# Kernel tuning notes

Hardware: AMD Instinct MI355X
Metric: run time of the kernel (lower is better)

## Reference

```python
import jax, jax.numpy as jnp
import numpy as np

GAMMA = 5e-4
IN_DIM, HID = 512, 4096
N = HID  # batch must equal hidden_dim for classifier(gram) to type-check


def setup_inputs() -> dict:
    key = jax.random.key(0)
    ks = jax.random.split(key, 7)
    s = lambda fan_in: 1.0 / np.sqrt(fan_in)
    return {
        "x": jax.random.normal(ks[0], (N, IN_DIM), jnp.float32),
        "W1": jax.random.uniform(ks[1], (HID, IN_DIM), jnp.float32, -s(IN_DIM), s(IN_DIM)),
        "b1": jax.random.uniform(ks[2], (HID,), jnp.float32, -s(IN_DIM), s(IN_DIM)),
        "W2": jax.random.uniform(ks[3], (HID, HID), jnp.float32, -s(HID), s(HID)),
        "b2": jax.random.uniform(ks[4], (HID,), jnp.float32, -s(HID), s(HID)),
        "Wc": jax.random.uniform(ks[5], (1, HID), jnp.float32, -s(HID), s(HID)),
        "bc": jax.random.uniform(ks[6], (1,), jnp.float32, -s(HID), s(HID)),
    }


def reference(x, W1, b1, W2, b2, Wc, bc):
    h = jnp.tanh(x @ W1.T + b1)          # [N, HID]
    h = jnp.tanh(h @ W2.T + b2)          # [N, HID]
    # KernelLayer: support = h.detach() (first call), RBF gram via cdist+exp
    support = jax.lax.stop_gradient(h)   # [N, HID]
    sq = (jnp.sum(h * h, axis=1, keepdims=True)
          + jnp.sum(support * support, axis=1)[None, :]
          - 2.0 * (h @ support.T))       # [N, N] squared distances
    gram = jnp.exp(-GAMMA * sq)
    return gram @ Wc.T + bc              # [N, 1]
```

## Files before the change

kernel.cpp:

```cpp
#include <hip/hip_runtime.h>
#include <hip/hip_bf16.h>


#define NROWS 4096
#define HID   4096
#define INDIM 512
#define GAMMA_F 5e-4f

typedef float f32x4  __attribute__((ext_vector_type(4)));
typedef int   i32x4  __attribute__((ext_vector_type(4)));
typedef int   i32x8  __attribute__((ext_vector_type(8)));

#define BAR() asm volatile("s_barrier" ::: "memory")
#define SCALE1 0x7F7F7F7F

__device__ __forceinline__ unsigned char f2e4m3(float x) {
  unsigned int u = __float_as_uint(x);
  unsigned char s = (unsigned char)((u >> 24) & 0x80u);
  float a = fabsf(x);
  if (a >= 448.f) return s | 0x7E;
  if (a < 0.015625f) {
    int q = (int)rintf(a * 512.f);
    return s | (unsigned char)q;
  }
  unsigned int ua = u & 0x7fffffffu;
  ua += 0x7FFFFu + ((ua >> 20) & 1u);
  int e = (int)(ua >> 23) - 127;
  unsigned int m = (ua >> 20) & 7u;
  return s | (unsigned char)(((e + 7) << 3) | m);
}

__global__ void prep(const float* __restrict__ x, const float* __restrict__ W1,
                     const float* __restrict__ W2, const float* __restrict__ bc,
                     unsigned char* __restrict__ xq, unsigned char* __restrict__ w1q,
                     unsigned char* __restrict__ w2q,
                     float* __restrict__ out, float* __restrict__ norms) {
  const int gi = blockIdx.x * blockDim.x + threadIdx.x;
  if (gi < NROWS) { out[gi] = bc[0]; norms[gi] = 0.f; }
  const int NX  = NROWS * INDIM / 8;
  const int NW2 = HID * HID / 8;
  const int total = 2 * NX + NW2;
  const int stride = gridDim.x * blockDim.x;
  for (int i = gi; i < total; i += stride) {
    const float* src; unsigned char* dst; float sc; int j;
    if (i < NX)            { src = x;  dst = xq;  sc = 16.f;  j = i; }
    else if (i < 2 * NX)   { src = W1; dst = w1q; sc = 32.f;  j = i - NX; }
    else                   { src = W2; dst = w2q; sc = 128.f; j = i - 2 * NX; }
    float4 v0 = ((const float4*)src)[j * 2];
    float4 v1 = ((const float4*)src)[j * 2 + 1];
    unsigned int r0 = (unsigned int)f2e4m3(v0.x * sc)
                    | ((unsigned int)f2e4m3(v0.y * sc) << 8)
                    | ((unsigned int)f2e4m3(v0.z * sc) << 16)
                    | ((unsigned int)f2e4m3(v0.w * sc) << 24);
    unsigned int r1 = (unsigned int)f2e4m3(v1.x * sc)
                    | ((unsigned int)f2e4m3(v1.y * sc) << 8)
                    | ((unsigned int)f2e4m3(v1.z * sc) << 16)
                    | ((unsigned int)f2e4m3(v1.w * sc) << 24);
    uint2 o; o.x = r0; o.y = r1;
    ((uint2*)dst)[j] = o;
  }
}

__device__ __forceinline__ void gload16(const void* g, void* l) {
  __builtin_amdgcn_global_load_lds(
      (const __attribute__((address_space(1))) void*)g,
      (__attribute__((address_space(3))) void*)l, 16, 0, 0);
}

#define LDFRAG(dst, base0, off, RSTRIDE) do {                       \
    i32x4 lo_ = *(const i32x4*)((base0) + (off));                   \
    i32x4 hi_ = *(const i32x4*)((base0) + (RSTRIDE) + (off));       \
    dst = __builtin_shufflevector(lo_, hi_, 0, 1, 2, 3, 4, 5, 6, 7); } while (0)

#define MFMA16(d, a, b) \
    d = __builtin_amdgcn_mfma_scale_f32_16x16x128_f8f6f4( \
        a, b, d, 0, 0, 0, SCALE1, 0, SCALE1)

template <int EPI>
__global__ __launch_bounds__(512, 2)
void gemm256_fp8(const unsigned char* __restrict__ A, const unsigned char* __restrict__ B,
                 int K, int N,
                 const float* __restrict__ bias, unsigned char* __restrict__ Hout,
                 float* __restrict__ norms_out) {
  __shared__ __align__(16) unsigned char As[2][2][256 * 64];
  __shared__ __align__(16) unsigned char Bs[2][2][256 * 64];

  const int tid  = threadIdx.x;
  const int lane = tid & 63;
  const int wave = tid >> 6;
  const int wr = wave >> 2, wc = wave & 3;
  const int fr = lane & 15, fq = lane >> 4;

  const int nwg = gridDim.x;
  const int cpx = nwg >> 3;
  const int bid = blockIdx.x;
  const int swzb = (bid & 7) * cpx + (bid >> 3);
  const int nbx = N >> 8;
  const int brow = (swzb / nbx) << 8;
  const int bcol = (swzb % nbx) << 8;

  const unsigned char* ap[4]; const unsigned char* bp[4]; int ldq[4];
#pragma unroll
  for (int q = 0; q < 4; ++q) {
    int idx = q * 512 + tid;
    int h   = idx >> 10;
    int row = (idx >> 2) & 255;
    int c   = idx & 3;
    int gcol = ((((c ^ ((row >> 1) & 3)) << 1) | h) << 4);
    ap[q] = A + (size_t)(brow + row) * K + gcol;
    bp[q] = B + (size_t)(bcol + row) * K + gcol;
    ldq[q] = (q * 512 + wave * 64) * 16;
  }
#define STAGE_A(p, tt) do { int kk = (tt) * 128;              \
    gload16(ap[0] + kk, &As[p][0][0] + ldq[0]);               \
    gload16(ap[1] + kk, &As[p][0][0] + ldq[1]);               \
    gload16(ap[2] + kk, &As[p][0][0] + ldq[2]);               \
    gload16(ap[3] + kk, &As[p][0][0] + ldq[3]); } while (0)
#define STAGE_B(p, tt) do { int kk = (tt) * 128;              \
    gload16(bp[0] + kk, &Bs[p][0][0] + ldq[0]);               \
    gload16(bp[1] + kk, &Bs[p][0][0] + ldq[1]);               \
    gload16(bp[2] + kk, &Bs[p][0][0] + ldq[2]);               \
    gload16(bp[3] + kk, &Bs[p][0][0] + ldq[3]); } while (0)

  int aoff[8], boff[4];
#pragma unroll
  for (int mi = 0; mi < 8; ++mi) {
    int row = wr * 128 + mi * 16 + fr;
    aoff[mi] = row * 64 + ((fq ^ ((row >> 1) & 3)) << 4);
  }
#pragma unroll
  for (int nj = 0; nj < 4; ++nj) {
    int row = wc * 64 + nj * 16 + fr;
    boff[nj] = row * 64 + ((fq ^ ((row >> 1) & 3)) << 4);
  }

  const int NT = K >> 7;

  STAGE_A(0, 0); STAGE_B(0, 0);
  STAGE_A(1, 1); STAGE_B(1, 1);
  asm volatile("s_waitcnt vmcnt(8)" ::: "memory");
  BAR();

  f32x4 acc[8][4] = {};
  i32x8 afr[4], bfr[4];

  for (int t = 0; t < NT; ++t) {
    const int p = t & 1;
    int t2 = t + 2; if (t2 >= NT) t2 = NT - 1;

#pragma unroll
    for (int mi = 0; mi < 4; ++mi) LDFRAG(afr[mi], &As[p][0][0], aoff[mi], 16384);
#pragma unroll
    for (int nj = 0; nj < 4; ++nj) LDFRAG(bfr[nj], &Bs[p][0][0], boff[nj], 16384);
    asm volatile("s_waitcnt lgkmcnt(0)" ::: "memory");
    BAR();
    STAGE_B(p, t2);
    __builtin_amdgcn_sched_barrier(0);
    __builtin_amdgcn_s_setprio(1);
#pragma unroll
    for (int mi = 0; mi < 4; ++mi)
#pragma unroll
      for (int nj = 0; nj < 4; ++nj) MFMA16(acc[mi][nj], afr[mi], bfr[nj]);
    __builtin_amdgcn_s_setprio(0);

#pragma unroll
    for (int mi = 0; mi < 4; ++mi) LDFRAG(afr[mi], &As[p][0][0], aoff[4 + mi], 16384);
    asm volatile("s_waitcnt lgkmcnt(0)" ::: "memory");
    BAR();
    STAGE_A(p, t2);
    __builtin_amdgcn_sched_barrier(0);
    __builtin_amdgcn_s_setprio(1);
#pragma unroll
    for (int mi = 0; mi < 4; ++mi)
#pragma unroll
      for (int nj = 0; nj < 4; ++nj) MFMA16(acc[4 + mi][nj], afr[mi], bfr[nj]);
    __builtin_amdgcn_s_setprio(0);
    asm volatile("s_waitcnt vmcnt(8)" ::: "memory");
    BAR();
  }
  asm volatile("s_waitcnt vmcnt(0)" ::: "memory");

  const float rescale = (EPI == 0) ? (1.f / 512.f) : (1.f / 1024.f);
  float bv[4];
#pragma unroll
  for (int nj = 0; nj < 4; ++nj) bv[nj] = bias[bcol + wc * 64 + nj * 16 + fr];
#pragma unroll
  for (int mi = 0; mi < 8; ++mi) {
    int row0 = brow + wr * 128 + mi * 16 + fq * 4;
#pragma unroll
    for (int rr = 0; rr < 4; ++rr) {
      float ns = 0.f;
#pragma unroll
      for (int nj = 0; nj < 4; ++nj) {
        int col = bcol + wc * 64 + nj * 16 + fr;
        float v = tanhf(acc[mi][nj][rr] * rescale + bv[nj]);
        Hout[(size_t)(row0 + rr) * N + col] = f2e4m3(8.f * v);
        if (EPI == 2) ns += v * v;
      }
      if (EPI == 2) {
        ns += __shfl_xor(ns, 1);
        ns += __shfl_xor(ns, 2);
        ns += __shfl_xor(ns, 4);
        ns += __shfl_xor(ns, 8);
        if (fr == 0) atomicAdd(&norms_out[row0 + rr], ns);
      }
    }
  }
#undef STAGE_A
#undef STAGE_B
}

__global__ __launch_bounds__(256, 2)
void gram_tri(const unsigned char* __restrict__ H, int K,
              const float* __restrict__ norms, const float* __restrict__ Wc,
              float* __restrict__ out) {
  __shared__ __align__(16) unsigned char As[2][2][128 * 64];
  __shared__ __align__(16) unsigned char Bs[2][2][128 * 64];

  const int tid  = threadIdx.x;
  const int lane = tid & 63;
  const int wave = tid >> 6;
  const int wr = wave >> 1, wc = wave & 1;
  const int fr = lane & 15, fq = lane >> 4;

  const int bid = blockIdx.x;
  const int swzb = (bid & 7) * 66 + (bid >> 3);
  int I = (int)((sqrtf(8.0f * (float)swzb + 1.0f) - 1.0f) * 0.5f);
  while ((I + 1) * (I + 2) / 2 <= swzb) ++I;
  while (I * (I + 1) / 2 > swzb) --I;
  const int J = swzb - I * (I + 1) / 2;
  const int brow = I << 7, bcol = J << 7;
  const bool diag = (I == J);

  const unsigned char* ap[4]; const unsigned char* bp[4]; int ldq[4];
#pragma unroll
  for (int q = 0; q < 4; ++q) {
    int idx = q * 256 + tid;
    int h   = idx >> 9;
    int row = (idx >> 2) & 127;
    int c   = idx & 3;
    int gcol = ((((c ^ ((row >> 1) & 3)) << 1) | h) << 4);
    ap[q] = H + (size_t)(brow + row) * K + gcol;
    bp[q] = H + (size_t)(bcol + row) * K + gcol;
    ldq[q] = (q * 256 + wave * 64) * 16;
  }
#define GSTAGE_A(p, tt) do { int kk = (tt) * 128;             \
    gload16(ap[0] + kk, &As[p][0][0] + ldq[0]);               \
    gload16(ap[1] + kk, &As[p][0][0] + ldq[1]);               \
    gload16(ap[2] + kk, &As[p][0][0] + ldq[2]);               \
    gload16(ap[3] + kk, &As[p][0][0] + ldq[3]); } while (0)
#define GSTAGE_B(p, tt) do { int kk = (tt) * 128;             \
    gload16(bp[0] + kk, &Bs[p][0][0] + ldq[0]);               \
    gload16(bp[1] + kk, &Bs[p][0][0] + ldq[1]);               \
    gload16(bp[2] + kk, &Bs[p][0][0] + ldq[2]);               \
    gload16(bp[3] + kk, &Bs[p][0][0] + ldq[3]); } while (0)

  int aoff[4], boff[4];
#pragma unroll
  for (int mi = 0; mi < 4; ++mi) {
    int row = wr * 64 + mi * 16 + fr;
    aoff[mi] = row * 64 + ((fq ^ ((row >> 1) & 3)) << 4);
  }
#pragma unroll
  for (int nj = 0; nj < 4; ++nj) {
    int row = wc * 64 + nj * 16 + fr;
    boff[nj] = row * 64 + ((fq ^ ((row >> 1) & 3)) << 4);
  }

  const int NT = K >> 7;

  GSTAGE_A(0, 0); GSTAGE_B(0, 0);
  GSTAGE_A(1, 1); GSTAGE_B(1, 1);
  asm volatile("s_waitcnt vmcnt(8)" ::: "memory");
  BAR();

  f32x4 acc[4][4] = {};

  for (int t = 0; t < NT; ++t) {
    const int p = t & 1;
    int t2 = t + 2; if (t2 >= NT) t2 = NT - 1;

    i32x8 af[4], bf[4];
#pragma unroll
    for (int mi = 0; mi < 4; ++mi) LDFRAG(af[mi], &As[p][0][0], aoff[mi], 8192);
#pragma unroll
    for (int nj = 0; nj < 4; ++nj) LDFRAG(bf[nj], &Bs[p][0][0], boff[nj], 8192);
    asm volatile("s_waitcnt lgkmcnt(0)" ::: "memory");
    BAR();
    GSTAGE_A(p, t2); GSTAGE_B(p, t2);
    __builtin_amdgcn_sched_barrier(0);
    __builtin_amdgcn_s_setprio(1);
#pragma unroll
    for (int mi = 0; mi < 4; ++mi)
#pragma unroll
      for (int nj = 0; nj < 4; ++nj) MFMA16(acc[mi][nj], af[mi], bf[nj]);
    __builtin_amdgcn_s_setprio(0);
    asm volatile("s_waitcnt vmcnt(8)" ::: "memory");
    BAR();
  }
  asm volatile("s_waitcnt vmcnt(0)" ::: "memory");

  float ncol[4], wcv[4];
#pragma unroll
  for (int nj = 0; nj < 4; ++nj) {
    int col = bcol + wc * 64 + nj * 16 + fr;
    ncol[nj] = norms[col];
    wcv[nj]  = Wc[col];
  }
  float colpart[4] = {0.f, 0.f, 0.f, 0.f};
#pragma unroll
  for (int mi = 0; mi < 4; ++mi) {
    int row0 = brow + wr * 64 + mi * 16 + fq * 4;
    float4 nr4  = *(const float4*)&norms[row0];
    float4 wcr4 = *(const float4*)&Wc[row0];
#pragma unroll
    for (int rr = 0; rr < 4; ++rr) {
      float nrow = (rr == 0) ? nr4.x : (rr == 1) ? nr4.y : (rr == 2) ? nr4.z : nr4.w;
      float wrow = (rr == 0) ? wcr4.x : (rr == 1) ? wcr4.y : (rr == 2) ? wcr4.z : wcr4.w;
      float rowpart = 0.f;
#pragma unroll
      for (int nj = 0; nj < 4; ++nj) {
        float sq = nrow + ncol[nj] - acc[mi][nj][rr] * 0.03125f;
        float e = __expf(-GAMMA_F * sq);
        rowpart += e * wcv[nj];
        colpart[nj] += e * wrow;
      }
      rowpart += __shfl_xor(rowpart, 1);
      rowpart += __shfl_xor(rowpart, 2);
      rowpart += __shfl_xor(rowpart, 4);
      rowpart += __shfl_xor(rowpart, 8);
      if (fr == 0) atomicAdd(&out[row0 + rr], rowpart);
    }
  }
  if (!diag) {
#pragma unroll
    for (int nj = 0; nj < 4; ++nj) {
      colpart[nj] += __shfl_xor(colpart[nj], 16);
      colpart[nj] += __shfl_xor(colpart[nj], 32);
      if (fq == 0) atomicAdd(&out[bcol + wc * 64 + nj * 16 + fr], colpart[nj]);
    }
  }
#undef GSTAGE_A
#undef GSTAGE_B
}

extern "C" void kernel_launch(void* const* d_in, const int* in_sizes, int n_in,
                              void* d_out, int out_size, void* d_ws, size_t ws_size,
                              hipStream_t stream) {
  const float* x  = (const float*)d_in[0];
  const float* W1 = (const float*)d_in[1];
  const float* b1 = (const float*)d_in[2];
  const float* W2 = (const float*)d_in[3];
  const float* b2 = (const float*)d_in[4];
  const float* Wc = (const float*)d_in[5];
  const float* bc = (const float*)d_in[6];
  float* out = (float*)d_out;

  char* ws = (char*)d_ws;
  unsigned char* xq  = (unsigned char*)ws; ws += (size_t)NROWS * INDIM;
  unsigned char* w1q = (unsigned char*)ws; ws += (size_t)HID * INDIM;
  unsigned char* w2q = (unsigned char*)ws; ws += (size_t)HID * HID;
  unsigned char* h1q = (unsigned char*)ws; ws += (size_t)NROWS * HID;
  unsigned char* h2q = (unsigned char*)ws; ws += (size_t)NROWS * HID;
  float* norms = (float*)ws;                ws += (size_t)NROWS * 4;

  prep<<<2048, 256, 0, stream>>>(x, W1, W2, bc, xq, w1q, w2q, out, norms);

  const int grid = (NROWS / 256) * (HID / 256);

  gemm256_fp8<0><<<grid, 512, 0, stream>>>(xq, w1q, INDIM, HID, b1, h1q, nullptr);
  gemm256_fp8<2><<<grid, 512, 0, stream>>>(h1q, w2q, HID, HID, b2, h2q, norms);
  gram_tri<<<528, 256, 0, stream>>>(h2q, HID, norms, Wc, out);
}
```

Before: 209.2 us.

## Restructure FP8 GEMM main loop into unrolled tile steps; simplify gram staging

The 256x256 FP8 GEMM loop becomes a templated two-step `tile_step`, unrolled by two. Each step loads all eight A fragments and four B fragments with compile-time LDS offsets, then issues the next-stage global-to-LDS copies for A and B together between the two MFMA halves. The aim is to cut address arithmetic and register shuffling in the hot loop. The gram kernel drops its double-buffered async pipeline for a single buffer bracketed by `__syncthreads`, so its global loads no longer overlap with MFMA work. The GEMM prefetch pointers now advance without clamping at the end of K, so the last iterations read past the tile and possibly past the end of the buffer.

```diff
diff --git a/kernel.cpp b/kernel.cpp
--- a/kernel.cpp
+++ b/kernel.cpp
@@ -13,6 +13,10 @@
 
 #define BAR() asm volatile("s_barrier" ::: "memory")
 #define SCALE1 0x7F7F7F7F
+
+#define MFMA16(d, a, b) \
+    d = __builtin_amdgcn_mfma_scale_f32_16x16x128_f8f6f4( \
+        a, b, d, 0, 0, 0, SCALE1, 0, SCALE1)
 
 __device__ __forceinline__ unsigned char f2e4m3(float x) {
   unsigned int u = __float_as_uint(x);
@@ -43,9 +47,9 @@
   const int stride = gridDim.x * blockDim.x;
   for (int i = gi; i < total; i += stride) {
     const float* src; unsigned char* dst; float sc; int j;
-    if (i < NX)            { src = x;  dst = xq;  sc = 16.f;  j = i; }
-    else if (i < 2 * NX)   { src = W1; dst = w1q; sc = 32.f;  j = i - NX; }
-    else                   { src = W2; dst = w2q; sc = 128.f; j = i - 2 * NX; }
+    if (i < NX)          { src = x;  dst = xq;  sc = 16.f;  j = i; }
+    else if (i < 2 * NX) { src = W1; dst = w1q; sc = 32.f;  j = i - NX; }
+    else                 { src = W2; dst = w2q; sc = 128.f; j = i - 2 * NX; }
     float4 v0 = ((const float4*)src)[j * 2];
     float4 v1 = ((const float4*)src)[j * 2 + 1];
     unsigned int r0 = (unsigned int)f2e4m3(v0.x * sc)
@@ -67,14 +71,47 @@
       (__attribute__((address_space(3))) void*)l, 16, 0, 0);
 }
 
-#define LDFRAG(dst, base0, off, RSTRIDE) do {                       \
-    i32x4 lo_ = *(const i32x4*)((base0) + (off));                   \
-    i32x4 hi_ = *(const i32x4*)((base0) + (RSTRIDE) + (off));       \
-    dst = __builtin_shufflevector(lo_, hi_, 0, 1, 2, 3, 4, 5, 6, 7); } while (0)
-
-#define MFMA16(d, a, b) \
-    d = __builtin_amdgcn_mfma_scale_f32_16x16x128_f8f6f4( \
-        a, b, d, 0, 0, 0, SCALE1, 0, SCALE1)
+template <int P, int SOFF>
+__device__ __forceinline__ void tile_step(
+    const unsigned char* Ard, const unsigned char* Brd,
+    const unsigned char* const* aq, const unsigned char* const* bq,
+    unsigned char* lA, unsigned char* lB, const int* lo,
+    f32x4 (*acc)[4]) {
+  i32x8 a[8], b[4];
+#pragma unroll
+  for (int mi = 0; mi < 8; ++mi) {
+    i32x4 l_ = *(const i32x4*)(Ard + P * 32768 + mi * 1024);
+    i32x4 h_ = *(const i32x4*)(Ard + P * 32768 + 16384 + mi * 1024);
+    a[mi] = __builtin_shufflevector(l_, h_, 0, 1, 2, 3, 4, 5, 6, 7);
+  }
+#pragma unroll
+  for (int nj = 0; nj < 4; ++nj) {
+    i32x4 l_ = *(const i32x4*)(Brd + P * 32768 + nj * 1024);
+    i32x4 h_ = *(const i32x4*)(Brd + P * 32768 + 16384 + nj * 1024);
+    b[nj] = __builtin_shufflevector(l_, h_, 0, 1, 2, 3, 4, 5, 6, 7);
+  }
+  __builtin_amdgcn_s_setprio(1);
+#pragma unroll
+  for (int mi = 0; mi < 4; ++mi)
+#pragma unroll
+    for (int nj = 0; nj < 4; ++nj) MFMA16(acc[mi][nj], a[mi], b[nj]);
+  __builtin_amdgcn_s_setprio(0);
+  asm volatile("s_waitcnt lgkmcnt(0)" ::: "memory");
+  BAR();
+#pragma unroll
+  for (int q = 0; q < 4; ++q) {
+    gload16(aq[q] + SOFF, lA + P * 32768 + lo[q]);
+    gload16(bq[q] + SOFF, lB + P * 32768 + lo[q]);
+  }
+  __builtin_amdgcn_s_setprio(1);
+#pragma unroll
+  for (int mi = 0; mi < 4; ++mi)
+#pragma unroll
+    for (int nj = 0; nj < 4; ++nj) MFMA16(acc[4 + mi][nj], a[4 + mi], b[nj]);
+  __builtin_amdgcn_s_setprio(0);
+  asm volatile("s_waitcnt vmcnt(8)" ::: "memory");
+  BAR();
+}
 
 template <int EPI>
 __global__ __launch_bounds__(512, 2)
@@ -99,7 +136,7 @@
   const int brow = (swzb / nbx) << 8;
   const int bcol = (swzb % nbx) << 8;
 
-  const unsigned char* ap[4]; const unsigned char* bp[4]; int ldq[4];
+  const unsigned char* aq[4]; const unsigned char* bq[4]; int lo[4];
 #pragma unroll
   for (int q = 0; q < 4; ++q) {
     int idx = q * 512 + tid;
@@ -107,76 +144,34 @@
     int row = (idx >> 2) & 255;
     int c   = idx & 3;
     int gcol = ((((c ^ ((row >> 1) & 3)) << 1) | h) << 4);
-    ap[q] = A + (size_t)(brow + row) * K + gcol;
-    bp[q] = B + (size_t)(bcol + row) * K + gcol;
-    ldq[q] = (q * 512 + wave * 64) * 16;
-  }
-#define STAGE_A(p, tt) do { int kk = (tt) * 128;              \
-    gload16(ap[0] + kk, &As[p][0][0] + ldq[0]);               \
-    gload16(ap[1] + kk, &As[p][0][0] + ldq[1]);               \
-    gload16(ap[2] + kk, &As[p][0][0] + ldq[2]);               \
-    gload16(ap[3] + kk, &As[p][0][0] + ldq[3]); } while (0)
-#define STAGE_B(p, tt) do { int kk = (tt) * 128;              \
-    gload16(bp[0] + kk, &Bs[p][0][0] + ldq[0]);               \
-    gload16(bp[1] + kk, &Bs[p][0][0] + ldq[1]);               \
-    gload16(bp[2] + kk, &Bs[p][0][0] + ldq[2]);               \
-    gload16(bp[3] + kk, &Bs[p][0][0] + ldq[3]); } while (0)
-
-  int aoff[8], boff[4];
-#pragma unroll
-  for (int mi = 0; mi < 8; ++mi) {
-    int row = wr * 128 + mi * 16 + fr;
-    aoff[mi] = row * 64 + ((fq ^ ((row >> 1) & 3)) << 4);
-  }
-#pragma unroll
-  for (int nj = 0; nj < 4; ++nj) {
-    int row = wc * 64 + nj * 16 + fr;
-    boff[nj] = row * 64 + ((fq ^ ((row >> 1) & 3)) << 4);
-  }
-
-  const int NT = K >> 7;
-
-  STAGE_A(0, 0); STAGE_B(0, 0);
-  STAGE_A(1, 1); STAGE_B(1, 1);
+    aq[q] = A + (size_t)(brow + row) * K + gcol;
+    bq[q] = B + (size_t)(bcol + row) * K + gcol;
+    lo[q] = wave * 1024 + q * 8192;
+  }
+  unsigned char* lA = &As[0][0][0];
+  unsigned char* lB = &Bs[0][0][0];
+
+  const int swz = (fr >> 1) & 3;
+  const unsigned char* Ard = lA + (wr * 128 + fr) * 64 + ((fq ^ swz) << 4);
+  const unsigned char* Brd = lB + (wc * 64 + fr) * 64 + ((fq ^ swz) << 4);
+
+#pragma unroll
+  for (int q = 0; q < 4; ++q) { gload16(aq[q], lA + lo[q]); gload16(bq[q], lB + lo[q]); }
+#pragma unroll
+  for (int q = 0; q < 4; ++q) { gload16(aq[q] + 128, lA + 32768 + lo[q]); gload16(bq[q] + 128, lB + 32768 + lo[q]); }
+#pragma unroll
+  for (int q = 0; q < 4; ++q) { aq[q] += 256; bq[q] += 256; }
   asm volatile("s_waitcnt vmcnt(8)" ::: "memory");
   BAR();
 
   f32x4 acc[8][4] = {};
-  i32x8 afr[4], bfr[4];
-
-  for (int t = 0; t < NT; ++t) {
-    const int p = t & 1;
-    int t2 = t + 2; if (t2 >= NT) t2 = NT - 1;
-
-#pragma unroll
-    for (int mi = 0; mi < 4; ++mi) LDFRAG(afr[mi], &As[p][0][0], aoff[mi], 16384);
-#pragma unroll
-    for (int nj = 0; nj < 4; ++nj) LDFRAG(bfr[nj], &Bs[p][0][0], boff[nj], 16384);
-    asm volatile("s_waitcnt lgkmcnt(0)" ::: "memory");
-    BAR();
-    STAGE_B(p, t2);
-    __builtin_amdgcn_sched_barrier(0);
-    __builtin_amdgcn_s_setprio(1);
-#pragma unroll
-    for (int mi = 0; mi < 4; ++mi)
-#pragma unroll
-      for (int nj = 0; nj < 4; ++nj) MFMA16(acc[mi][nj], afr[mi], bfr[nj]);
-    __builtin_amdgcn_s_setprio(0);
-
-#pragma unroll
-    for (int mi = 0; mi < 4; ++mi) LDFRAG(afr[mi], &As[p][0][0], aoff[4 + mi], 16384);
-    asm volatile("s_waitcnt lgkmcnt(0)" ::: "memory");
-    BAR();
-    STAGE_A(p, t2);
-    __builtin_amdgcn_sched_barrier(0);
-    __builtin_amdgcn_s_setprio(1);
-#pragma unroll
-    for (int mi = 0; mi < 4; ++mi)
-#pragma unroll
-      for (int nj = 0; nj < 4; ++nj) MFMA16(acc[4 + mi][nj], afr[mi], bfr[nj]);
-    __builtin_amdgcn_s_setprio(0);
-    asm volatile("s_waitcnt vmcnt(8)" ::: "memory");
-    BAR();
+
+  const int NT = K >> 7;
+  for (int t = 0; t < NT; t += 2) {
+    tile_step<0, 0>(Ard, Brd, aq, bq, lA, lB, lo, acc);
+    tile_step<1, 128>(Ard, Brd, aq, bq, lA, lB, lo, acc);
+#pragma unroll
+    for (int q = 0; q < 4; ++q) { aq[q] += 256; bq[q] += 256; }
   }
   asm volatile("s_waitcnt vmcnt(0)" ::: "memory");
 
@@ -206,16 +201,14 @@
       }
     }
   }
-#undef STAGE_A
-#undef STAGE_B
 }
 
 __global__ __launch_bounds__(256, 2)
 void gram_tri(const unsigned char* __restrict__ H, int K,
               const float* __restrict__ norms, const float* __restrict__ Wc,
               float* __restrict__ out) {
-  __shared__ __align__(16) unsigned char As[2][2][128 * 64];
-  __shared__ __align__(16) unsigned char Bs[2][2][128 * 64];
+  __shared__ __align__(16) unsigned char As[2][128 * 64];
+  __shared__ __align__(16) unsigned char Bs[2][128 * 64];
 
   const int tid  = threadIdx.x;
   const int lane = tid & 63;
@@ -244,16 +237,6 @@
     bp[q] = H + (size_t)(bcol + row) * K + gcol;
     ldq[q] = (q * 256 + wave * 64) * 16;
   }
-#define GSTAGE_A(p, tt) do { int kk = (tt) * 128;             \
-    gload16(ap[0] + kk, &As[p][0][0] + ldq[0]);               \
-    gload16(ap[1] + kk, &As[p][0][0] + ldq[1]);               \
-    gload16(ap[2] + kk, &As[p][0][0] + ldq[2]);               \
-    gload16(ap[3] + kk, &As[p][0][0] + ldq[3]); } while (0)
-#define GSTAGE_B(p, tt) do { int kk = (tt) * 128;             \
-    gload16(bp[0] + kk, &Bs[p][0][0] + ldq[0]);               \
-    gload16(bp[1] + kk, &Bs[p][0][0] + ldq[1]);               \
-    gload16(bp[2] + kk, &Bs[p][0][0] + ldq[2]);               \
-    gload16(bp[3] + kk, &Bs[p][0][0] + ldq[3]); } while (0)
 
   int aoff[4], boff[4];
 #pragma unroll
@@ -267,38 +250,41 @@
     boff[nj] = row * 64 + ((fq ^ ((row >> 1) & 3)) << 4);
   }
 
-  const int NT = K >> 7;
-
-  GSTAGE_A(0, 0); GSTAGE_B(0, 0);
-  GSTAGE_A(1, 1); GSTAGE_B(1, 1);
-  asm volatile("s_waitcnt vmcnt(8)" ::: "memory");
-  BAR();
+#define LDFRAG(dst, base0, off) do {                                \
+    i32x4 lo_ = *(const i32x4*)((base0) + (off));                   \
+    i32x4 hi_ = *(const i32x4*)((base0) + 8192 + (off));            \
+    dst = __builtin_shufflevector(lo_, hi_, 0, 1, 2, 3, 4, 5, 6, 7); } while (0)
 
   f32x4 acc[4][4] = {};
 
-  for (int t = 0; t < NT; ++t) {
-    const int p = t & 1;
-    int t2 = t + 2; if (t2 >= NT) t2 = NT - 1;
+  for (int t = 0; t < (K >> 7); ++t) {
+    __syncthreads();
+    {
+      int kk = t * 128;
+      gload16(ap[0] + kk, &As[0][0] + ldq[0]);
+      gload16(ap[1] + kk, &As[0][0] + ldq[1]);
+      gload16(ap[2] + kk, &As[0][0] + ldq[2]);
+      gload16(ap[3] + kk, &As[0][0] + ldq[3]);
+      gload16(bp[0] + kk, &Bs[0][0] + ldq[0]);
+      gload16(bp[1] + kk, &Bs[0][0] + ldq[1]);
+      gload16(bp[2] + kk, &Bs[0][0] + ldq[2]);
+      gload16(bp[3] + kk, &Bs[0][0] + ldq[3]);
+    }
+    __syncthreads();
 
     i32x8 af[4], bf[4];
 #pragma unroll
-    for (int mi = 0; mi < 4; ++mi) LDFRAG(af[mi], &As[p][0][0], aoff[mi], 8192);
-#pragma unroll
-    for (int nj = 0; nj < 4; ++nj) LDFRAG(bf[nj], &Bs[p][0][0], boff[nj], 8192);
-    asm volatile("s_waitcnt lgkmcnt(0)" ::: "memory");
-    BAR();
-    GSTAGE_A(p, t2); GSTAGE_B(p, t2);
-    __builtin_amdgcn_sched_barrier(0);
-    __builtin_amdgcn_s_setprio(1);
+    for (int mi = 0; mi < 4; ++mi) LDFRAG(af[mi], &As[0][0], aoff[mi]);
+#pragma unroll
+    for (int nj = 0; nj < 4; ++nj) LDFRAG(bf[nj], &Bs[0][0], boff[nj]);
 #pragma unroll
     for (int mi = 0; mi < 4; ++mi)
 #pragma unroll
-      for (int nj = 0; nj < 4; ++nj) MFMA16(acc[mi][nj], af[mi], bf[nj]);
-    __builtin_amdgcn_s_setprio(0);
-    asm volatile("s_waitcnt vmcnt(8)" ::: "memory");
-    BAR();
-  }
-  asm volatile("s_waitcnt vmcnt(0)" ::: "memory");
+      for (int nj = 0; nj < 4; ++nj)
+        acc[mi][nj] = __builtin_amdgcn_mfma_scale_f32_16x16x128_f8f6f4(
+            af[mi], bf[nj], acc[mi][nj], 0, 0, 0, SCALE1, 0, SCALE1);
+  }
+#undef LDFRAG
 
   float ncol[4], wcv[4];
 #pragma unroll
@@ -340,8 +326,6 @@
       if (fq == 0) atomicAdd(&out[bcol + wc * 64 + nj * 16 + fr], colpart[nj]);
     }
   }
-#undef GSTAGE_A
-#undef GSTAGE_B
 }
 
 extern "C" void kernel_launch(void* const* d_in, const int* in_sizes, int n_in,
```

Measured after the change: 479.3 us. 2.29x slower.

## Replace double-buffered prefetch in gram kernel with single-buffer synchronous loads

Applied to the files above, without the earlier changes.

The gram_tri kernel drops its two-stage LDS ring, where tile t+2 was prefetched while MFMAs ran on tile t. Each K step now loads its A/B tiles into one LDS buffer between two __syncthreads, then reads fragments and runs the MFMAs. This removes the hand-tuned waitcnt, sched_barrier and setprio code and halves LDS use. The cost is that global-load latency is no longer hidden behind compute, so the loop becomes load-then-compute serialized.

```diff
diff --git a/kernel.cpp b/kernel.cpp
--- a/kernel.cpp
+++ b/kernel.cpp
@@ -13,6 +13,10 @@
 
 #define BAR() asm volatile("s_barrier" ::: "memory")
 #define SCALE1 0x7F7F7F7F
+
+#define MFMA16(d, a, b) \
+    d = __builtin_amdgcn_mfma_scale_f32_16x16x128_f8f6f4( \
+        a, b, d, 0, 0, 0, SCALE1, 0, SCALE1)
 
 __device__ __forceinline__ unsigned char f2e4m3(float x) {
   unsigned int u = __float_as_uint(x);
@@ -43,9 +47,9 @@
   const int stride = gridDim.x * blockDim.x;
   for (int i = gi; i < total; i += stride) {
     const float* src; unsigned char* dst; float sc; int j;
-    if (i < NX)            { src = x;  dst = xq;  sc = 16.f;  j = i; }
-    else if (i < 2 * NX)   { src = W1; dst = w1q; sc = 32.f;  j = i - NX; }
-    else                   { src = W2; dst = w2q; sc = 128.f; j = i - 2 * NX; }
+    if (i < NX)          { src = x;  dst = xq;  sc = 16.f;  j = i; }
+    else if (i < 2 * NX) { src = W1; dst = w1q; sc = 32.f;  j = i - NX; }
+    else                 { src = W2; dst = w2q; sc = 128.f; j = i - 2 * NX; }
     float4 v0 = ((const float4*)src)[j * 2];
     float4 v1 = ((const float4*)src)[j * 2 + 1];
     unsigned int r0 = (unsigned int)f2e4m3(v0.x * sc)
@@ -71,10 +75,6 @@
     i32x4 lo_ = *(const i32x4*)((base0) + (off));                   \
     i32x4 hi_ = *(const i32x4*)((base0) + (RSTRIDE) + (off));       \
     dst = __builtin_shufflevector(lo_, hi_, 0, 1, 2, 3, 4, 5, 6, 7); } while (0)
-
-#define MFMA16(d, a, b) \
-    d = __builtin_amdgcn_mfma_scale_f32_16x16x128_f8f6f4( \
-        a, b, d, 0, 0, 0, SCALE1, 0, SCALE1)
 
 template <int EPI>
 __global__ __launch_bounds__(512, 2)
@@ -214,8 +214,8 @@
 void gram_tri(const unsigned char* __restrict__ H, int K,
               const float* __restrict__ norms, const float* __restrict__ Wc,
               float* __restrict__ out) {
-  __shared__ __align__(16) unsigned char As[2][2][128 * 64];
-  __shared__ __align__(16) unsigned char Bs[2][2][128 * 64];
+  __shared__ __align__(16) unsigned char As[2][128 * 64];
+  __shared__ __align__(16) unsigned char Bs[2][128 * 64];
 
   const int tid  = threadIdx.x;
   const int lane = tid & 63;
@@ -244,16 +244,6 @@
     bp[q] = H + (size_t)(bcol + row) * K + gcol;
     ldq[q] = (q * 256 + wave * 64) * 16;
   }
-#define GSTAGE_A(p, tt) do { int kk = (tt) * 128;             \
-    gload16(ap[0] + kk, &As[p][0][0] + ldq[0]);               \
-    gload16(ap[1] + kk, &As[p][0][0] + ldq[1]);               \
-    gload16(ap[2] + kk, &As[p][0][0] + ldq[2]);               \
-    gload16(ap[3] + kk, &As[p][0][0] + ldq[3]); } while (0)
-#define GSTAGE_B(p, tt) do { int kk = (tt) * 128;             \
-    gload16(bp[0] + kk, &Bs[p][0][0] + ldq[0]);               \
-    gload16(bp[1] + kk, &Bs[p][0][0] + ldq[1]);               \
-    gload16(bp[2] + kk, &Bs[p][0][0] + ldq[2]);               \
-    gload16(bp[3] + kk, &Bs[p][0][0] + ldq[3]); } while (0)
 
   int aoff[4], boff[4];
 #pragma unroll
@@ -267,38 +257,35 @@
     boff[nj] = row * 64 + ((fq ^ ((row >> 1) & 3)) << 4);
   }
 
-  const int NT = K >> 7;
-
-  GSTAGE_A(0, 0); GSTAGE_B(0, 0);
-  GSTAGE_A(1, 1); GSTAGE_B(1, 1);
-  asm volatile("s_waitcnt vmcnt(8)" ::: "memory");
-  BAR();
-
   f32x4 acc[4][4] = {};
 
-  for (int t = 0; t < NT; ++t) {
-    const int p = t & 1;
-    int t2 = t + 2; if (t2 >= NT) t2 = NT - 1;
+  for (int t = 0; t < (K >> 7); ++t) {
+    __syncthreads();
+    {
+      int kk = t * 128;
+      gload16(ap[0] + kk, &As[0][0] + ldq[0]);
+      gload16(ap[1] + kk, &As[0][0] + ldq[1]);
+      gload16(ap[2] + kk, &As[0][0] + ldq[2]);
+      gload16(ap[3] + kk, &As[0][0] + ldq[3]);
+      gload16(bp[0] + kk, &Bs[0][0] + ldq[0]);
+      gload16(bp[1] + kk, &Bs[0][0] + ldq[1]);
+      gload16(bp[2] + kk, &Bs[0][0] + ldq[2]);
+      gload16(bp[3] + kk, &Bs[0][0] + ldq[3]);
+    }
+    __syncthreads();
 
     i32x8 af[4], bf[4];
 #pragma unroll
-    for (int mi = 0; mi < 4; ++mi) LDFRAG(af[mi], &As[p][0][0], aoff[mi], 8192);
-#pragma unroll
-    for (int nj = 0; nj < 4; ++nj) LDFRAG(bf[nj], &Bs[p][0][0], boff[nj], 8192);
-    asm volatile("s_waitcnt lgkmcnt(0)" ::: "memory");
-    BAR();
-    GSTAGE_A(p, t2); GSTAGE_B(p, t2);
-    __builtin_amdgcn_sched_barrier(0);
-    __builtin_amdgcn_s_setprio(1);
+    for (int mi = 0; mi < 4; ++mi) LDFRAG(af[mi], &As[0][0], aoff[mi], 8192);
+#pragma unroll
+    for (int nj = 0; nj < 4; ++nj) LDFRAG(bf[nj], &Bs[0][0], boff[nj], 8192);
 #pragma unroll
     for (int mi = 0; mi < 4; ++mi)
 #pragma unroll
-      for (int nj = 0; nj < 4; ++nj) MFMA16(acc[mi][nj], af[mi], bf[nj]);
-    __builtin_amdgcn_s_setprio(0);
-    asm volatile("s_waitcnt vmcnt(8)" ::: "memory");
-    BAR();
-  }
-  asm volatile("s_waitcnt vmcnt(0)" ::: "memory");
+      for (int nj = 0; nj < 4; ++nj)
+        acc[mi][nj] = __builtin_amdgcn_mfma_scale_f32_16x16x128_f8f6f4(
+            af[mi], bf[nj], acc[mi][nj], 0, 0, 0, SCALE1, 0, SCALE1);
+  }
 
   float ncol[4], wcv[4];
 #pragma unroll
@@ -340,8 +327,6 @@
       if (fq == 0) atomicAdd(&out[bcol + wc * 64 + nj * 16 + fr], colpart[nj]);
     }
   }
-#undef GSTAGE_A
-#undef GSTAGE_B
 }
 
 extern "C" void kernel_launch(void* const* d_in, const int* in_sizes, int n_in,
```

Result: faster. 193.7 us (-7.4%).
